# Kernel tuning notes

Hardware: AMD Instinct MI355X
Metric: run time of the kernel (lower is better)

## Reference

```python
import jax, jax.numpy as jnp
import numpy as np
from jax import lax

# SLAYER neuron / simulation constants (netParams)
THETA = 1.0      # spike threshold
TAU_SR = 4.0     # PSP (SRM) kernel time constant
TAU_REF = 1.0    # refractory kernel time constant
SCALE_REF = 2.0  # refractory scale (kernel amplitude = -scaleRef*theta)
TAU_RHO = 1.0    # surrogate-gradient width (used in bwd only)
SCALE_RHO = 1.0

B, F_IN, T = 8, 6300, 500  # 6300 = 50*63*2
HID, OUT = 32, 20


def _alpha_scan(x, d):
    """Causal conv with alpha kernel k*d**k along last (time) axis via 2-state recurrence.
    x: [..., T]. y[t] = sum_{j<=t} x[j]*(t-j)*d**(t-j)."""
    xt = jnp.moveaxis(x, -1, 0)  # [T, ...]
    zero = jnp.zeros_like(xt[0])

    def step(carry, xi):
        z, y = carry
        y_new = d * (y + z)       # y[t] = d*(y[t-1] + z[t-1])
        z_new = d * z + xi        # z[t] = d*z[t-1] + x[t]
        return (z_new, y_new), y_new

    _, ys = lax.scan(step, (zero, zero), xt)
    return jnp.moveaxis(ys, 0, -1)


def psp(x):
    """SLAYER psp: convolve spike train with SRM kernel eps(k) = (k/tauSr)*exp(1-k/tauSr)."""
    d = float(np.exp(-1.0 / TAU_SR))
    return jnp.float32(np.e / TAU_SR) * _alpha_scan(x, d)


def _spike_impl(p):
    """Iterative threshold + refractory. p: [..., T] membrane input (post-psp, post-dense).
    Refractory kernel: ref(k) = -scaleRef*theta*(k/tauRef)*exp(1-k/tauRef), realized by the
    same 2-state alpha recurrence driven by emitted spikes."""
    d = float(np.exp(-1.0 / TAU_REF))
    C = jnp.float32(-SCALE_REF * THETA * np.e / TAU_REF)
    pt = jnp.moveaxis(p, -1, 0)  # [T, ...]
    zero = jnp.zeros_like(pt[0])

    def step(carry, pi):
        z, y = carry
        y_new = d * (y + z)                 # alpha state from past spikes (lag>=1)
        u = pi + C * y_new                  # membrane potential incl. refractory
        s = (u >= THETA).astype(pi.dtype)   # hard threshold
        z_new = d * z + s
        return (z_new, y_new), s

    _, ss = lax.scan(step, (zero, zero), pt)
    return jnp.moveaxis(ss, 0, -1)


def spike(p):
    return _spike_impl(p)


def setup_inputs() -> dict:
    key = jax.random.key(0)
    k1, k2, k3 = jax.random.split(key, 3)
    downsampled = (jax.random.uniform(k1, (B, F_IN, T)) < 0.05).astype(jnp.float32)
    w1 = jax.random.normal(k2, (HID, F_IN), jnp.float32) * 0.05
    w2 = jax.random.normal(k3, (OUT, HID), jnp.float32) * 0.3
    return {"downsampled": downsampled, "w1": w1, "w2": w2}


def reference(downsampled, w1, w2):
    # spike_1 = spike(psp(downsampled))
    s1 = spike(psp(downsampled))
    # spike_2 = spike(fc1(psp(spike_1)))
    s2 = spike(jnp.einsum('of,bft->bot', w1, psp(s1)))
    # spike_3 = spike(fc2(psp(spike_2)))
    s3 = spike(jnp.einsum('of,bft->bot', w2, psp(s2)))
    return s3
```

## Files before the change

### kernel.cpp

```cpp
#include <hip/hip_runtime.h>
#include <stdint.h>

#define NB 8
#define F_IN 6300
#define NT 500
#define HID 32
#define NOUT 20
#define NW 99
#define NWD 8

#define D_SR   0.7788007830714049f
#define S_SR   0.6795704571147613f
#define D_REF  0.36787944117144233f
#define C_REF  -5.43656365691809f

#define NROWB ((NB * F_IN) / 4)

__global__ __launch_bounds__(256) void k0_pack(const float* __restrict__ x,
                                               const float* __restrict__ w1,
                                               uint64_t* __restrict__ xb,
                                               float* __restrict__ w1t) {
  const int bid = blockIdx.x;
  const int tid = threadIdx.x;
  if (bid < NROWB) {
    const int row = bid * 4 + (tid >> 6);
    const int lane = tid & 63;
    const float* xr = x + (size_t)row * NT;
    uint64_t m[8];
#pragma unroll
    for (int k = 0; k < 8; k++) {
      int t = k * 64 + lane;
      float v = (t < NT) ? xr[t] : 0.f;
      m[k] = __ballot(v > 0.5f);
    }
    if (lane == 0) {
      uint64_t* dst = xb + (size_t)row * NWD;
#pragma unroll
      for (int k = 0; k < 8; k++) dst[k] = m[k];
    }
    return;
  }
  __shared__ float tl[64][33];
  const int f0 = (bid - NROWB) * 64;
  const int r = tid & 63, g = tid >> 6;
#pragma unroll
  for (int oo = 0; oo < 32; oo += 4) {
    int o = oo + g;
    int f = f0 + r;
    tl[r][o] = (f < F_IN) ? w1[o * F_IN + f] : 0.f;
  }
  __syncthreads();
#pragma unroll
  for (int k = 0; k < 8; k++) {
    int idx = k * 256 + tid;
    int rr = idx >> 5, cc = idx & 31;
    int f = f0 + rr;
    if (f < F_IN) w1t[(size_t)f * 32 + cc] = tl[rr][cc];
  }
}

__global__ __launch_bounds__(64, 1) void k1_layer1(const uint64_t* __restrict__ xb,
                                                   uint64_t* __restrict__ masks) {
  const int wi = blockIdx.x;
  const int b  = blockIdx.y;
  const int lane = threadIdx.x;
  const int f = wi * 64 + lane;
  const uint64_t vmask = __ballot(f < F_IN);
  const int fc = (f < F_IN) ? f : (F_IN - 1);
  const uint64_t* xr = xb + ((size_t)b * F_IN + fc) * NWD;
  uint64_t* mrow = masks + ((size_t)b * NW + wi) * NT;

  float y1 = 0.f, z1 = 0.f, yr = 0.f, zr = 0.f;
  uint64_t wcur = xr[0];

#pragma unroll 1
  for (int gg = 0; gg < 8; gg++) {
    const int gn = (gg < 7) ? gg + 1 : 7;
    uint64_t wnxt = xr[gn];
    const uint32_t wlo = (uint32_t)wcur;
    const uint32_t whi = (uint32_t)(wcur >> 32);
    uint64_t keep = 0;
#pragma unroll
    for (int j = 0; j < 64; j++) {
      const uint32_t bw = (j < 32) ? wlo : whi;
      const bool xbit = ((bw >> (j & 31)) & 1u) != 0u;
      float zm = __fmul_rn(D_SR, z1);
      y1 = __fmul_rn(D_SR, __fadd_rn(y1, z1));
      z1 = xbit ? __fadd_rn(zm, 1.0f) : zm;
      float p = __fmul_rn(S_SR, y1);
      yr = __fmul_rn(D_REF, __fadd_rn(yr, zr));
      float u = __fadd_rn(p, __fmul_rn(C_REF, yr));
      bool s = (u >= 1.0f);
      float zrm = __fmul_rn(D_REF, zr);
      zr = s ? __fadd_rn(zrm, 1.0f) : zrm;
      uint64_t mball = __ballot(s);
      if (lane == j) keep = mball;
    }
    uint64_t* mp = mrow + gg * 64;
    if (gg < 7)                 mp[lane] = keep & vmask;
    else if (lane < NT - 7*64)  mp[lane] = keep & vmask;
    wcur = wnxt;
  }
}

__global__ __launch_bounds__(512) void k2_fc1(const float* __restrict__ w1t,
                                              const uint64_t* __restrict__ masks,
                                              double* __restrict__ R) {
  __shared__ double part[8][32];
  const int tid = threadIdx.x;
  const int wv = tid >> 6;
  const int lane = tid & 63;
  const int half = lane >> 5;
  const int o = lane & 31;
  const int b = blockIdx.x;
  const int t = blockIdx.y * 4 + (wv & 3);
  const int seg = wv >> 2;
  const int wbeg = seg * 50, wend = seg ? NW : 50;
  const uint64_t* mbase = masks + (size_t)b * NW * NT + t;
  const char* wrow = (const char*)w1t + o * 4;
  double acc0 = 0.0, acc1 = 0.0, acc2 = 0.0, acc3 = 0.0;

  int wi = wbeg + half;
  uint64_t mcur = (wi < wend) ? mbase[(size_t)wi * NT] : 0;
  for (; wi < wend; wi += 2) {
    uint64_t mnext = (wi + 2 < wend) ? mbase[(size_t)(wi + 2) * NT] : 0;
    const uint32_t base0 = ((uint32_t)wi << 13);
    uint32_t w = (uint32_t)mcur;
    uint32_t boff = base0;
#pragma unroll
    for (int sub = 0; sub < 2; sub++) {
      while (w) {
        uint32_t i0 = __builtin_ctz(w);                 uint32_t w1_ = w & (w - 1);
        uint32_t i1 = w1_ ? __builtin_ctz(w1_) : 0u;    uint32_t w2_ = w1_ ? (w1_ & (w1_ - 1)) : 0u;
        uint32_t i2 = w2_ ? __builtin_ctz(w2_) : 0u;    uint32_t w3_ = w2_ ? (w2_ & (w2_ - 1)) : 0u;
        uint32_t i3 = w3_ ? __builtin_ctz(w3_) : 0u;    w = w3_ ? (w3_ & (w3_ - 1)) : 0u;
        float a0 = *(const float*)(wrow + boff + (i0 << 7));
        float a1 = *(const float*)(wrow + boff + (i1 << 7));
        float a2 = *(const float*)(wrow + boff + (i2 << 7));
        float a3 = *(const float*)(wrow + boff + (i3 << 7));
        a1 = w1_ ? a1 : 0.0f;
        a2 = w2_ ? a2 : 0.0f;
        a3 = w3_ ? a3 : 0.0f;
        acc0 += (double)a0;
        acc1 += (double)a1;
        acc2 += (double)a2;
        acc3 += (double)a3;
      }
      w = (uint32_t)(mcur >> 32);
      boff = base0 + (32u << 7);
    }
    mcur = mnext;
  }
  double acc = (acc0 + acc1) + (acc2 + acc3);
  int hi2 = __shfl_xor(__double2hiint(acc), 32);
  int lo2 = __shfl_xor(__double2loint(acc), 32);
  acc += __hiloint2double(hi2, lo2);
  if (half == 0) part[wv][o] = acc;
  __syncthreads();
  if (wv < 4 && half == 0) {
    double tot = part[wv][o] + part[wv + 4][o];
    R[((size_t)b * NT + t) * HID + o] = tot;
  }
}

#define SNN_FAST_STEP(rin, EMIT)                                                \
  {                                                                             \
    y2 = __builtin_fma(dsr, y2, w);                                   \
    z2 = __builtin_fma(dsr, z2, (rin));                               \
    w  = dsr * z2;                                                              \
    double p  = ssr * y2;                                                       \
    double u0 = __builtin_fma(cr, q, p);                                        \
    double u1 = u0 + K;                                                         \
    double u  = sp ? u1 : u0;                                                   \
    bool s = (u >= 1.0);                                                        \
    double yr = q + (sp ? dre : 0.0);                                 \
    double zr = zrd + (sp ? 1.0 : 0.0);                           \
    zrd = dre * zr;                                                             \
    q = __builtin_fma(dre, yr, dre * zrd);                             \
    sp = s;                                                                     \
    EMIT                                                                        \
  }

#define P1_GROUP(g, v0, v1, v2, v3)                                             \
  {                                                                             \
    const int t = (g) * 4;                                                      \
    SNN_FAST_STEP(v0, { uint32_t mm = (uint32_t)__ballot(s);                    \
      if (lane == 0) s2l[t] = mm; })                                            \
    SNN_FAST_STEP(v1, { uint32_t mm = (uint32_t)__ballot(s);                    \
      if (lane == 0) s2l[t + 1] = mm; })                                        \
    SNN_FAST_STEP(v2, { uint32_t mm = (uint32_t)__ballot(s);                    \
      if (lane == 0) s2l[t + 2] = mm; })                                        \
    SNN_FAST_STEP(v3, { uint32_t mm = (uint32_t)__ballot(s);                    \
      if (lane == 0) s2l[t + 3] = mm; })                                        \
  }

#define P3_GROUP(g, v0, v1, v2, v3)                                             \
  {                                                                             \
    float4 ov;                                                                  \
    SNN_FAST_STEP(v0, { ov.x = s ? 1.0f : 0.0f; })                              \
    SNN_FAST_STEP(v1, { ov.y = s ? 1.0f : 0.0f; })                              \
    SNN_FAST_STEP(v2, { ov.z = s ? 1.0f : 0.0f; })                              \
    SNN_FAST_STEP(v3, { ov.w = s ? 1.0f : 0.0f; })                              \
    *(float4*)(orow + (g) * 4) = ov;                                            \
  }

__global__ __launch_bounds__(512, 1) void k345(const float* __restrict__ w2,
                                               const double* __restrict__ R,
                                               float* __restrict__ out) {
  __shared__ float    w2l[NOUT * 33];
  __shared__ uint32_t s2l[NT];
  __shared__ double   r3l[NT * NOUT];
  const int b = blockIdx.x;
  const int tid = threadIdx.x;
  const int lane = tid & 63;
  const int wv = tid >> 6;

  for (int i = tid; i < NOUT * HID; i += 512) w2l[(i >> 5) * 33 + (i & 31)] = w2[i];

  const double dsr = (double)D_SR, ssr = (double)S_SR;
  const double dre = (double)D_REF, cr = (double)C_REF;
  const double K = cr * dre;

  if (wv == 0 && lane < 32) {
    const double* Rb = R + (size_t)b * NT * HID + lane;
    double y2 = 0, z2 = 0, w = 0, q = 0, zrd = 0;
    bool sp = false;

    double buf[8][4];
#pragma unroll
    for (int j = 0; j < 8; j++)
#pragma unroll
      for (int e = 0; e < 4; e++) buf[j][e] = Rb[(size_t)(j * 4 + e) * HID];

#pragma unroll 1
    for (int g8 = 0; g8 < 15; g8++) {
#pragma unroll
      for (int j = 0; j < 8; j++) {
        const int g = g8 * 8 + j;
        double v0 = buf[j][0], v1 = buf[j][1], v2 = buf[j][2], v3 = buf[j][3];
        int gp = g + 8;
        if (gp > 124) gp = 124;
#pragma unroll
        for (int e = 0; e < 4; e++) buf[j][e] = Rb[((size_t)gp * 4 + e) * HID];
        P1_GROUP(g, v0, v1, v2, v3)
      }
    }
#pragma unroll
    for (int j = 0; j < 5; j++) {
      const int g = 120 + j;
      double v0 = buf[j][0], v1 = buf[j][1], v2 = buf[j][2], v3 = buf[j][3];
      P1_GROUP(g, v0, v1, v2, v3)
    }
  }
  __syncthreads();

#pragma unroll 1
  for (int base = 0; base < NT * NOUT; base += 512) {
    int task = base + tid;
    if (task < NT * NOUT) {
      int o = task % NOUT;
      int t = task / NOUT;
      uint32_t m = s2l[t];
      const float* wr = w2l + o * 33;
      double acc = 0.0;
      while (m) {
        uint32_t i0 = __builtin_ctz(m);                 uint32_t m1_ = m & (m - 1);
        uint32_t i1 = m1_ ? __builtin_ctz(m1_) : 0u;    uint32_t m2_ = m1_ ? (m1_ & (m1_ - 1)) : 0u;
        uint32_t i2 = m2_ ? __builtin_ctz(m2_) : 0u;    uint32_t m3_ = m2_ ? (m2_ & (m2_ - 1)) : 0u;
        uint32_t i3 = m3_ ? __builtin_ctz(m3_) : 0u;    m = m3_ ? (m3_ & (m3_ - 1)) : 0u;
        float a0 = wr[i0];
        float a1 = m1_ ? wr[i1] : 0.0f;
        float a2 = m2_ ? wr[i2] : 0.0f;
        float a3 = m3_ ? wr[i3] : 0.0f;
        acc += (double)a0;
        acc += (double)a1;
        acc += (double)a2;
        acc += (double)a3;
      }
      r3l[t * NOUT + o] = acc;
    }
  }
  __syncthreads();

  if (wv == 0 && lane < NOUT) {
    const int o = lane;
    float* orow = out + ((size_t)b * NOUT + o) * NT;
    double y2 = 0, z2 = 0, w = 0, q = 0, zrd = 0;
    bool sp = false;

    double c0 = r3l[0 * NOUT + o], c1 = r3l[1 * NOUT + o];
    double c2 = r3l[2 * NOUT + o], c3 = r3l[3 * NOUT + o];
#pragma unroll 1
    for (int g = 0; g < 125; g++) {
      const int gp = (g < 124) ? g + 1 : 124;
      double n0 = r3l[(gp * 4 + 0) * NOUT + o];
      double n1 = r3l[(gp * 4 + 1) * NOUT + o];
      double n2 = r3l[(gp * 4 + 2) * NOUT + o];
      double n3 = r3l[(gp * 4 + 3) * NOUT + o];
      P3_GROUP(g, c0, c1, c2, c3)
      c0 = n0; c1 = n1; c2 = n2; c3 = n3;
    }
  }
}

extern "C" void kernel_launch(void* const* d_in, const int* in_sizes, int n_in,
                              void* d_out, int out_size, void* d_ws, size_t ws_size,
                              hipStream_t stream) {
  const float* x  = (const float*)d_in[0];
  const float* w1 = (const float*)d_in[1];
  const float* w2 = (const float*)d_in[2];
  float* out = (float*)d_out;

  uint8_t* ws = (uint8_t*)d_ws;
  const size_t W1T_BYTES  = (size_t)F_IN * HID * 4;
  const size_t XBF_BYTES  = (size_t)NB * F_IN * NWD * 8;
  const size_t MASK_BYTES = (size_t)NB * NW * NT * 8;
  float*    w1t   = (float*)ws;
  uint64_t* xbF   = (uint64_t*)(ws + W1T_BYTES);
  uint64_t* masks = (uint64_t*)(ws + W1T_BYTES + XBF_BYTES);
  double*   R     = (double*)(ws + W1T_BYTES + XBF_BYTES + MASK_BYTES);

  k0_pack<<<NROWB + 99, 256, 0, stream>>>(x, w1, xbF, w1t);
  k1_layer1<<<dim3(NW, NB), 64, 0, stream>>>(xbF, masks);
  k2_fc1<<<dim3(NB, NT / 4), 512, 0, stream>>>(w1t, masks, R);
  k345<<<NB, 512, 0, stream>>>(w2, R, out);
}
```

Before: 310.5 us.

## Parallelize PSP alpha-scan in k345 via chunked two-pass scan

Replaces the serial per-timestep PSP recurrence inside the layer-2 and layer-3 spike loops with a chunked parallel scan. Each time axis is split into 16 chunks of 32 steps: local chunk states are computed in parallel, then combined serially with a 32-step decay carry (DL = dsr^32), and a final pass writes PSP values to shared memory. The serial spike loops then only run the refractory threshold recurrence. This shortens the per-step critical path at the cost of extra shared memory (a 128 KB p2l buffer), reading R twice, and more block-wide syncs.

```diff
diff --git a/kernel.cpp b/kernel.cpp
--- a/kernel.cpp
+++ b/kernel.cpp
@@ -163,93 +163,101 @@
   }
 }
 
-#define SNN_FAST_STEP(rin, EMIT)                                                \
+#define REF_STEP(pin, EMIT)                                                     \
   {                                                                             \
-    y2 = __builtin_fma(dsr, y2, w);                                   \
-    z2 = __builtin_fma(dsr, z2, (rin));                               \
-    w  = dsr * z2;                                                              \
-    double p  = ssr * y2;                                                       \
-    double u0 = __builtin_fma(cr, q, p);                                        \
+    double u0 = __builtin_fma(cr, q, (pin));                                    \
     double u1 = u0 + K;                                                         \
     double u  = sp ? u1 : u0;                                                   \
     bool s = (u >= 1.0);                                                        \
-    double yr = q + (sp ? dre : 0.0);                                 \
-    double zr = zrd + (sp ? 1.0 : 0.0);                           \
+    double yr = q + (sp ? dre : 0.0);                                           \
+    double zr = zrd + (sp ? 1.0 : 0.0);                                         \
     zrd = dre * zr;                                                             \
-    q = __builtin_fma(dre, yr, dre * zrd);                             \
+    q = __builtin_fma(dre, yr, dre * zrd);                                      \
     sp = s;                                                                     \
     EMIT                                                                        \
-  }
-
-#define P1_GROUP(g, v0, v1, v2, v3)                                             \
-  {                                                                             \
-    const int t = (g) * 4;                                                      \
-    SNN_FAST_STEP(v0, { uint32_t mm = (uint32_t)__ballot(s);                    \
-      if (lane == 0) s2l[t] = mm; })                                            \
-    SNN_FAST_STEP(v1, { uint32_t mm = (uint32_t)__ballot(s);                    \
-      if (lane == 0) s2l[t + 1] = mm; })                                        \
-    SNN_FAST_STEP(v2, { uint32_t mm = (uint32_t)__ballot(s);                    \
-      if (lane == 0) s2l[t + 2] = mm; })                                        \
-    SNN_FAST_STEP(v3, { uint32_t mm = (uint32_t)__ballot(s);                    \
-      if (lane == 0) s2l[t + 3] = mm; })                                        \
-  }
-
-#define P3_GROUP(g, v0, v1, v2, v3)                                             \
-  {                                                                             \
-    float4 ov;                                                                  \
-    SNN_FAST_STEP(v0, { ov.x = s ? 1.0f : 0.0f; })                              \
-    SNN_FAST_STEP(v1, { ov.y = s ? 1.0f : 0.0f; })                              \
-    SNN_FAST_STEP(v2, { ov.z = s ? 1.0f : 0.0f; })                              \
-    SNN_FAST_STEP(v3, { ov.w = s ? 1.0f : 0.0f; })                              \
-    *(float4*)(orow + (g) * 4) = ov;                                            \
   }
 
 __global__ __launch_bounds__(512, 1) void k345(const float* __restrict__ w2,
                                                const double* __restrict__ R,
                                                float* __restrict__ out) {
+  __shared__ double   p2l[NT * HID];
+  __shared__ double   zcl[16 * HID], ycl[16 * HID];
+  __shared__ double   zil[16 * HID], yil[16 * HID];
   __shared__ float    w2l[NOUT * 33];
   __shared__ uint32_t s2l[NT];
-  __shared__ double   r3l[NT * NOUT];
+  double* r3l = p2l;
+
   const int b = blockIdx.x;
   const int tid = threadIdx.x;
-  const int lane = tid & 63;
-  const int wv = tid >> 6;
-
-  for (int i = tid; i < NOUT * HID; i += 512) w2l[(i >> 5) * 33 + (i & 31)] = w2[i];
 
   const double dsr = (double)D_SR, ssr = (double)S_SR;
   const double dre = (double)D_REF, cr = (double)C_REF;
   const double K = cr * dre;
-
-  if (wv == 0 && lane < 32) {
-    const double* Rb = R + (size_t)b * NT * HID + lane;
-    double y2 = 0, z2 = 0, w = 0, q = 0, zrd = 0;
+  const double DL = 3.3546262790251185e-4;
+
+  for (int i = tid; i < NOUT * HID; i += 512) w2l[(i >> 5) * 33 + (i & 31)] = w2[i];
+
+  {
+    const int h = tid & 31;
+    const int k = tid >> 5;
+    const int t0 = k * 32;
+    const int L = (k == 15) ? (NT - 480) : 32;
+    const double* Rb = R + (size_t)b * NT * HID + h;
+    double z = 0.0, y = 0.0;
+    for (int i = 0; i < L; i++) {
+      double x = Rb[(size_t)(t0 + i) * HID];
+      y = dsr * (y + z);
+      z = __builtin_fma(dsr, z, x);
+    }
+    zcl[k * HID + h] = z; ycl[k * HID + h] = y;
+  }
+  __syncthreads();
+  if (tid < HID) {
+    const int h = tid;
+    double z = 0.0, y = 0.0;
+    for (int k = 0; k < 16; k++) {
+      zil[k * HID + h] = z; yil[k * HID + h] = y;
+      double zc = zcl[k * HID + h], yc = ycl[k * HID + h];
+      y = __builtin_fma(DL, __builtin_fma(32.0, z, y), yc);
+      z = __builtin_fma(DL, z, zc);
+    }
+  }
+  __syncthreads();
+  {
+    const int h = tid & 31;
+    const int k = tid >> 5;
+    const int t0 = k * 32;
+    const int L = (k == 15) ? (NT - 480) : 32;
+    const double* Rb = R + (size_t)b * NT * HID + h;
+    double z = zil[k * HID + h], y = yil[k * HID + h];
+    for (int i = 0; i < L; i++) {
+      double x = Rb[(size_t)(t0 + i) * HID];
+      y = dsr * (y + z);
+      z = __builtin_fma(dsr, z, x);
+      p2l[(t0 + i) * HID + h] = ssr * y;
+    }
+  }
+  __syncthreads();
+
+  if (tid < 32) {
+    const int h = tid;
+    double q = 0.0, zrd = 0.0;
     bool sp = false;
-
-    double buf[8][4];
-#pragma unroll
-    for (int j = 0; j < 8; j++)
-#pragma unroll
-      for (int e = 0; e < 4; e++) buf[j][e] = Rb[(size_t)(j * 4 + e) * HID];
-
+    double c0 = p2l[0 * HID + h], c1 = p2l[1 * HID + h];
+    double c2 = p2l[2 * HID + h], c3 = p2l[3 * HID + h];
 #pragma unroll 1
-    for (int g8 = 0; g8 < 15; g8++) {
-#pragma unroll
-      for (int j = 0; j < 8; j++) {
-        const int g = g8 * 8 + j;
-        double v0 = buf[j][0], v1 = buf[j][1], v2 = buf[j][2], v3 = buf[j][3];
-        int gp = g + 8;
-        if (gp > 124) gp = 124;
-#pragma unroll
-        for (int e = 0; e < 4; e++) buf[j][e] = Rb[((size_t)gp * 4 + e) * HID];
-        P1_GROUP(g, v0, v1, v2, v3)
-      }
-    }
-#pragma unroll
-    for (int j = 0; j < 5; j++) {
-      const int g = 120 + j;
-      double v0 = buf[j][0], v1 = buf[j][1], v2 = buf[j][2], v3 = buf[j][3];
-      P1_GROUP(g, v0, v1, v2, v3)
+    for (int g = 0; g < 125; g++) {
+      const int gp = (g < 124) ? g + 1 : 124;
+      double n0 = p2l[(gp * 4 + 0) * HID + h];
+      double n1 = p2l[(gp * 4 + 1) * HID + h];
+      double n2 = p2l[(gp * 4 + 2) * HID + h];
+      double n3 = p2l[(gp * 4 + 3) * HID + h];
+      const int t = g * 4;
+      REF_STEP(c0, { uint32_t mm = (uint32_t)__ballot(s); if (h == 0) s2l[t] = mm; })
+      REF_STEP(c1, { uint32_t mm = (uint32_t)__ballot(s); if (h == 0) s2l[t + 1] = mm; })
+      REF_STEP(c2, { uint32_t mm = (uint32_t)__ballot(s); if (h == 0) s2l[t + 2] = mm; })
+      REF_STEP(c3, { uint32_t mm = (uint32_t)__ballot(s); if (h == 0) s2l[t + 3] = mm; })
+      c0 = n0; c1 = n1; c2 = n2; c3 = n3;
     }
   }
   __syncthreads();
@@ -282,12 +290,52 @@
   }
   __syncthreads();
 
-  if (wv == 0 && lane < NOUT) {
-    const int o = lane;
+  if (tid < 16 * NOUT) {
+    const int o = tid % NOUT;
+    const int k = tid / NOUT;
+    const int t0 = k * 32;
+    const int L = (k == 15) ? (NT - 480) : 32;
+    double z = 0.0, y = 0.0;
+    for (int i = 0; i < L; i++) {
+      double x = r3l[(t0 + i) * NOUT + o];
+      y = dsr * (y + z);
+      z = __builtin_fma(dsr, z, x);
+    }
+    zcl[k * NOUT + o] = z; ycl[k * NOUT + o] = y;
+  }
+  __syncthreads();
+  if (tid < NOUT) {
+    const int o = tid;
+    double z = 0.0, y = 0.0;
+    for (int k = 0; k < 16; k++) {
+      zil[k * NOUT + o] = z; yil[k * NOUT + o] = y;
+      double zc = zcl[k * NOUT + o], yc = ycl[k * NOUT + o];
+      y = __builtin_fma(DL, __builtin_fma(32.0, z, y), yc);
+      z = __builtin_fma(DL, z, zc);
+    }
+  }
+  __syncthreads();
+  if (tid < 16 * NOUT) {
+    const int o = tid % NOUT;
+    const int k = tid / NOUT;
+    const int t0 = k * 32;
+    const int L = (k == 15) ? (NT - 480) : 32;
+    double z = zil[k * NOUT + o], y = yil[k * NOUT + o];
+    for (int i = 0; i < L; i++) {
+      const int idx = (t0 + i) * NOUT + o;
+      double x = r3l[idx];
+      y = dsr * (y + z);
+      z = __builtin_fma(dsr, z, x);
+      r3l[idx] = ssr * y;
+    }
+  }
+  __syncthreads();
+
+  if (tid < NOUT) {
+    const int o = tid;
     float* orow = out + ((size_t)b * NOUT + o) * NT;
-    double y2 = 0, z2 = 0, w = 0, q = 0, zrd = 0;
+    double q = 0.0, zrd = 0.0;
     bool sp = false;
-
     double c0 = r3l[0 * NOUT + o], c1 = r3l[1 * NOUT + o];
     double c2 = r3l[2 * NOUT + o], c3 = r3l[3 * NOUT + o];
 #pragma unroll 1
@@ -297,7 +345,12 @@
       double n1 = r3l[(gp * 4 + 1) * NOUT + o];
       double n2 = r3l[(gp * 4 + 2) * NOUT + o];
       double n3 = r3l[(gp * 4 + 3) * NOUT + o];
-      P3_GROUP(g, c0, c1, c2, c3)
+      float4 ov;
+      REF_STEP(c0, { ov.x = s ? 1.0f : 0.0f; })
+      REF_STEP(c1, { ov.y = s ? 1.0f : 0.0f; })
+      REF_STEP(c2, { ov.z = s ? 1.0f : 0.0f; })
+      REF_STEP(c3, { ov.w = s ? 1.0f : 0.0f; })
+      *(float4*)(orow + g * 4) = ov;
       c0 = n0; c1 = n1; c2 = n2; c3 = n3;
     }
   }
```

Result: no change. 316.4 us (+1.9%).
